# Kernel tuning notes

Hardware: AMD Instinct MI355X
Metric: run time of the kernel (lower is better)

Reference implementation:

```python
import jax, jax.numpy as jnp
import numpy as np

B, T, C, H = 2, 2048, 1024, 16
HD = C // H  # head dim = 64


def setup_inputs() -> dict:
    key = jax.random.key(0)
    ks = jax.random.split(key, 9)
    s = 1.0 / np.sqrt(C)
    return {
        "x": jax.random.normal(ks[0], (B, T, C), dtype=jnp.float32),
        "Wq": jax.random.normal(ks[1], (C, C), dtype=jnp.float32) * s,
        "bq": jax.random.normal(ks[2], (C,), dtype=jnp.float32) * 0.02,
        "Wk": jax.random.normal(ks[3], (C, C), dtype=jnp.float32) * s,
        "bk": jax.random.normal(ks[4], (C,), dtype=jnp.float32) * 0.02,
        "Wv": jax.random.normal(ks[5], (C, C), dtype=jnp.float32) * s,
        "bv": jax.random.normal(ks[6], (C,), dtype=jnp.float32) * 0.02,
        "Wo": jax.random.normal(ks[7], (C, C), dtype=jnp.float32) * s,
        "bo": jax.random.normal(ks[8], (C,), dtype=jnp.float32) * 0.02,
    }


def reference(x, Wq, bq, Wk, bk, Wv, bv, Wo, bo):
    # Projections (torch Linear: x @ W.T + b; here W stored pre-transposed as [C_in, C_out])
    q = x @ Wq + bq  # (B,T,C)
    k = x @ Wk + bk
    v = x @ Wv + bv
    # Split heads: (B,T,C) -> (B,H,T,HD)
    q = q.reshape(B, T, H, HD).transpose(0, 2, 1, 3)
    k = k.reshape(B, T, H, HD).transpose(0, 2, 1, 3)
    v = v.reshape(B, T, H, HD).transpose(0, 2, 1, 3)
    # NOTE: original module never applies a causal mask despite its name.
    score = jnp.einsum("bhqd,bhkd->bhqk", q, k) / jnp.sqrt(jnp.float32(HD))
    score = jax.nn.softmax(score, axis=-1)
    y = jnp.einsum("bhqk,bhkd->bhqd", score, v)
    y = y.transpose(0, 2, 1, 3).reshape(B, T, C)
    # dropout is identity in eval mode
    return y @ Wo + bo
```

## Files before the change

### kernel.cpp

```cpp
#include <hip/hip_runtime.h>
#include <math.h>

#define B_ 2
#define T_ 2048
#define C_ 1024
#define H_ 16
#define HD_ 64
#define M_ (B_*T_)

typedef _Float16 half2v __attribute__((ext_vector_type(2)));
typedef _Float16 half4v __attribute__((ext_vector_type(4)));
typedef _Float16 half8v __attribute__((ext_vector_type(8)));
typedef float f32x4 __attribute__((ext_vector_type(4)));

#define GLD_LDS(gp, lp) \
  __builtin_amdgcn_global_load_lds( \
      (const __attribute__((address_space(1))) void*)(gp), \
      (__attribute__((address_space(3))) void*)(lp), 16, 0, 0)

__global__ __launch_bounds__(256) void cast_f16_kernel(
    const float* __restrict__ src, _Float16* __restrict__ dst, int n4)
{
  int i = blockIdx.x * 256 + threadIdx.x;
  if (i < n4) {
    float4 v = ((const float4*)src)[i];
    half4v h; h[0] = (_Float16)v.x; h[1] = (_Float16)v.y;
    h[2] = (_Float16)v.z; h[3] = (_Float16)v.w;
    ((half4v*)dst)[i] = h;
  }
}

__global__ __launch_bounds__(256) void transpose_cast_all_kernel(
    const float* __restrict__ Wq, const float* __restrict__ Wk,
    const float* __restrict__ Wv, const float* __restrict__ Wo,
    _Float16* __restrict__ Wt3, _Float16* __restrict__ Wot)
{
  const float* W; _Float16* Wt;
  switch (blockIdx.z) {
    case 0:  W = Wq; Wt = Wt3; break;
    case 1:  W = Wk; Wt = Wt3 + (size_t)1024 * 1024; break;
    case 2:  W = Wv; Wt = Wt3 + (size_t)2048 * 1024; break;
    default: W = Wo; Wt = Wot; break;
  }
  __shared__ float tile[32][33];
  const int tx = threadIdx.x, ty = threadIdx.y;
  const int n0 = blockIdx.x * 32, k0 = blockIdx.y * 32;
#pragma unroll
  for (int r = 0; r < 4; r++) {
    int k = ty + r * 8;
    tile[k][tx] = W[(size_t)(k0 + k) * C_ + n0 + tx];
  }
  __syncthreads();
#pragma unroll
  for (int r = 0; r < 4; r++) {
    int n = ty + r * 8;
    Wt[(size_t)(n0 + n) * C_ + k0 + tx] = (_Float16)tile[tx][n];
  }
}

__global__ __launch_bounds__(256) void concat_bias_kernel(
    const float* __restrict__ bq, const float* __restrict__ bk,
    const float* __restrict__ bv, float* __restrict__ b3)
{
  int i = blockIdx.x * 256 + threadIdx.x;
  const float* s = (i < 1024) ? bq : ((i < 2048) ? bk : bv);
  b3[i] = s[i & 1023];
}

template <int BM, int BN, int EPI>
__global__ __launch_bounds__(256) void gemm_f16_kernel(
    const _Float16* __restrict__ A, const _Float16* __restrict__ Bw,
    const float* __restrict__ bias,
    _Float16* __restrict__ o0, _Float16* __restrict__ o1,
    _Float16* __restrict__ o2, float* __restrict__ of)
{
  constexpr int FM = BM / 32, FN = BN / 32;
  __shared__ __align__(16) _Float16 As[BM * 32];
  __shared__ __align__(16) _Float16 Bs[BN * 32];
  const int t = threadIdx.x;
  const int w = t >> 6, lane = t & 63, l15 = lane & 15, quad = lane >> 4;
  const int wm = (w & 1) * (BM / 2), wn = (w >> 1) * (BN / 2);
  const int bm = blockIdx.y * BM, bn = blockIdx.x * BN;
  const int lrow = lane >> 2, lcol = (lane & 3) * 8;

  f32x4 acc[FM][FN];
#pragma unroll
  for (int i = 0; i < FM; i++)
#pragma unroll
    for (int j = 0; j < FN; j++) acc[i][j] = (f32x4){0.f, 0.f, 0.f, 0.f};

  for (int k0 = 0; k0 < 1024; k0 += 32) {
#pragma unroll
    for (int i = 0; i < BM / 64; i++) {
      int ca = w + 4 * i;
      int row = ca * 16 + lrow;
      GLD_LDS(A + (size_t)(bm + row) * 1024 + k0 + lcol, As + ca * 512);
    }
#pragma unroll
    for (int i = 0; i < BN / 64; i++) {
      int cb = w + 4 * i;
      int row = cb * 16 + lrow;
      GLD_LDS(Bw + (size_t)(bn + row) * 1024 + k0 + lcol, Bs + cb * 512);
    }
    __syncthreads();

    half8v af[FM], bf[FN];
#pragma unroll
    for (int mt = 0; mt < FM; mt++)
      af[mt] = *(const half8v*)(As + (wm + mt * 16 + l15) * 32 + quad * 8);
#pragma unroll
    for (int nt = 0; nt < FN; nt++)
      bf[nt] = *(const half8v*)(Bs + (wn + nt * 16 + l15) * 32 + quad * 8);
#pragma unroll
    for (int mt = 0; mt < FM; mt++)
#pragma unroll
      for (int nt = 0; nt < FN; nt++)
        acc[mt][nt] = __builtin_amdgcn_mfma_f32_16x16x32_f16(
            af[mt], bf[nt], acc[mt][nt], 0, 0, 0);
    __syncthreads();
  }

#pragma unroll
  for (int mt = 0; mt < FM; mt++)
#pragma unroll
    for (int nt = 0; nt < FN; nt++) {
      int n = bn + wn + nt * 16 + l15;
      float bv = bias[n];
#pragma unroll
      for (int r = 0; r < 4; r++) {
        int m = bm + wm + mt * 16 + quad * 4 + r;
        float v = acc[mt][nt][r] + bv;
        if (EPI == 0) {
          if (bn < 1024) {
            o0[(size_t)m * 1024 + n] = (_Float16)(v * 0.180336884f);
          } else if (bn < 2048) {
            o1[(size_t)m * 1024 + (n - 1024)] = (_Float16)v;
          } else {
            int dg = n - 2048;
            int hh = dg >> 6, hd = dg & 63;
            int bb = m >> 11, tt = m & 2047;
            o2[(((size_t)(bb * H_ + hh)) * 64 + hd) * 2048 + tt] = (_Float16)v;
          }
        } else {
          of[(size_t)m * 1024 + n] = v;
        }
      }
    }
}

__global__ __launch_bounds__(256) void attn_f16_kernel(
    const _Float16* __restrict__ Qh, const _Float16* __restrict__ Kh,
    const _Float16* __restrict__ Vt, _Float16* __restrict__ Yh)
{
  __shared__ __align__(16) _Float16 Ks[64 * 68];
  __shared__ __align__(16) _Float16 Vs[64 * 68];
  const int t = threadIdx.x;
  const int w = t >> 6, lane = t & 63, l15 = lane & 15, quad = lane >> 4;
  const int qt = blockIdx.x, h = blockIdx.y, b = blockIdx.z;
  const int qg = qt * 64 + w * 16 + l15;
  const size_t qoff = ((size_t)(b * T_ + qg)) * C_ + h * HD_;

  half8v qf[2];
  qf[0] = *(const half8v*)(Qh + qoff + quad * 8);
  qf[1] = *(const half8v*)(Qh + qoff + 32 + quad * 8);

  f32x4 o[4];
#pragma unroll
  for (int i = 0; i < 4; i++) o[i] = (f32x4){0.f, 0.f, 0.f, 0.f};
  float m_run = -INFINITY, l_run = 0.f;

  const size_t kbase = ((size_t)b * T_) * C_ + h * HD_;
  const size_t vbase = ((size_t)(b * H_ + h)) * HD_ * 2048;

  const int srow = t >> 3, scp = t & 7;

  for (int kt0 = 0; kt0 < T_; kt0 += 64) {
#pragma unroll
    for (int i = 0; i < 2; i++) {
      int row = srow + i * 32;
      *(uint4*)((char*)Ks + row * 136 + scp * 16) =
          *(const uint4*)(Kh + kbase + (size_t)(kt0 + row) * C_ + scp * 8);
      *(uint4*)((char*)Vs + row * 136 + scp * 16) =
          *(const uint4*)(Vt + vbase + (size_t)row * 2048 + kt0 + scp * 8);
    }
    __syncthreads();

    f32x4 s[4];
#pragma unroll
    for (int kt = 0; kt < 4; kt++) {
      s[kt] = (f32x4){0.f, 0.f, 0.f, 0.f};
      int key = kt * 16 + l15;
#pragma unroll
      for (int ks = 0; ks < 2; ks++) {
        half8v kf = *(const half8v*)((char*)Ks + key * 136 + (ks * 4 + quad) * 16);
        s[kt] = __builtin_amdgcn_mfma_f32_16x16x32_f16(kf, qf[ks], s[kt], 0, 0, 0);
      }
    }

    float tmax = -INFINITY;
#pragma unroll
    for (int kt = 0; kt < 4; kt++)
#pragma unroll
      for (int r = 0; r < 4; r++) tmax = fmaxf(tmax, s[kt][r]);
    tmax = fmaxf(tmax, __shfl_xor(tmax, 16));
    tmax = fmaxf(tmax, __shfl_xor(tmax, 32));
    float mnew = fmaxf(m_run, tmax);
    float alpha = __builtin_amdgcn_exp2f(m_run - mnew);

    float psum = 0.f;
    half4v pf[4];
#pragma unroll
    for (int kt = 0; kt < 4; kt++) {
      float p0 = __builtin_amdgcn_exp2f(s[kt][0] - mnew);
      float p1 = __builtin_amdgcn_exp2f(s[kt][1] - mnew);
      float p2 = __builtin_amdgcn_exp2f(s[kt][2] - mnew);
      float p3 = __builtin_amdgcn_exp2f(s[kt][3] - mnew);
      psum += (p0 + p1) + (p2 + p3);
      half2v pk01 = __builtin_bit_cast(half2v, __builtin_amdgcn_cvt_pkrtz(p0, p1));
      half2v pk23 = __builtin_bit_cast(half2v, __builtin_amdgcn_cvt_pkrtz(p2, p3));
      pf[kt] = __builtin_shufflevector(pk01, pk23, 0, 1, 2, 3);
    }
    psum += __shfl_xor(psum, 16);
    psum += __shfl_xor(psum, 32);
    l_run = l_run * alpha + psum;
    m_run = mnew;
#pragma unroll
    for (int dt = 0; dt < 4; dt++) o[dt] *= alpha;

#pragma unroll
    for (int dt = 0; dt < 4; dt++) {
      int d = dt * 16 + l15;
#pragma unroll
      for (int kt = 0; kt < 4; kt++) {
        half4v vf = *(const half4v*)((char*)Vs + d * 136 + kt * 32 + quad * 8);
        o[dt] = __builtin_amdgcn_mfma_f32_16x16x16f16(vf, pf[kt], o[dt], 0, 0, 0);
      }
    }
    __syncthreads();
  }

  float inv = 1.0f / l_run;
#pragma unroll
  for (int dt = 0; dt < 4; dt++) {
    half4v yv;
#pragma unroll
    for (int r = 0; r < 4; r++) yv[r] = (_Float16)(o[dt][r] * inv);
    *(half4v*)(Yh + qoff + dt * 16 + quad * 4) = yv;
  }
}

extern "C" void kernel_launch(void* const* d_in, const int* in_sizes, int n_in,
                              void* d_out, int out_size, void* d_ws, size_t ws_size,
                              hipStream_t stream) {
  const float* x  = (const float*)d_in[0];
  const float* Wq = (const float*)d_in[1];
  const float* bq = (const float*)d_in[2];
  const float* Wk = (const float*)d_in[3];
  const float* bk = (const float*)d_in[4];
  const float* Wv = (const float*)d_in[5];
  const float* bv = (const float*)d_in[6];
  const float* Wo = (const float*)d_in[7];
  const float* bo = (const float*)d_in[8];
  float* out = (float*)d_out;

  char* ws = (char*)d_ws;
  _Float16* xh   = (_Float16*)(ws);
  _Float16* Qh   = (_Float16*)(ws + (((size_t)8)  << 20));
  _Float16* Kh   = (_Float16*)(ws + (((size_t)16) << 20));
  _Float16* Vt   = (_Float16*)(ws + (((size_t)24) << 20));
  _Float16* Yh   = (_Float16*)(ws + (((size_t)32) << 20));
  _Float16* Wt3  = (_Float16*)(ws + (((size_t)40) << 20));
  _Float16* Wot  = (_Float16*)(ws + (((size_t)46) << 20));
  float*    b3   = (float*)   (ws + (((size_t)48) << 20));

  cast_f16_kernel<<<(M_ * C_ / 4 + 255) / 256, 256, 0, stream>>>(x, xh, M_ * C_ / 4);
  transpose_cast_all_kernel<<<dim3(32, 32, 4), dim3(32, 8), 0, stream>>>(
      Wq, Wk, Wv, Wo, Wt3, Wot);
  concat_bias_kernel<<<12, 256, 0, stream>>>(bq, bk, bv, b3);

  gemm_f16_kernel<128, 128, 0><<<dim3(24, 32), 256, 0, stream>>>(
      xh, Wt3, b3, Qh, Kh, Vt, nullptr);

  attn_f16_kernel<<<dim3(T_ / 64, H_, B_), 256, 0, stream>>>(Qh, Kh, Vt, Yh);

  gemm_f16_kernel<64, 128, 1><<<dim3(8, 64), 256, 0, stream>>>(
      Yh, Wot, bo, nullptr, nullptr, nullptr, out);
}
```

Before: 223.1 us.

## Double-buffer attention K/V tiles, lazy softmax rescale, separate V transpose kernel

```diff
diff --git a/kernel.cpp b/kernel.cpp
--- a/kernel.cpp
+++ b/kernel.cpp
@@ -65,6 +65,35 @@
   int i = blockIdx.x * 256 + threadIdx.x;
   const float* s = (i < 1024) ? bq : ((i < 2048) ? bk : bv);
   b3[i] = s[i & 1023];
+}
+
+__global__ __launch_bounds__(256) void transpose_v_kernel(
+    const _Float16* __restrict__ Vh, _Float16* __restrict__ Vt)
+{
+  __shared__ __align__(16) _Float16 tile[64 * 64];
+  const int tid = threadIdx.x;
+  const int t0 = blockIdx.x * 64;
+  const int bb = blockIdx.y >> 4, hh = blockIdx.y & 15;
+#pragma unroll
+  for (int i = 0; i < 2; i++) {
+    int slot = tid + i * 256;
+    int row_t = slot >> 3, cp = slot & 7;
+    uint4 v = *(const uint4*)(Vh + (size_t)(bb * T_ + t0 + row_t) * C_ +
+                              hh * 64 + cp * 8);
+    half8v hv = __builtin_bit_cast(half8v, v);
+    int c = ((row_t >> 3) ^ cp) * 8 + (row_t & 7);
+#pragma unroll
+    for (int j = 0; j < 8; j++)
+      tile[(cp * 8 + j) * 64 + c] = hv[j];
+  }
+  __syncthreads();
+#pragma unroll
+  for (int i = 0; i < 2; i++) {
+    int slot = tid + i * 256;
+    int d_row = slot >> 3, tc = slot & 7;
+    uint4 v = *(const uint4*)(tile + d_row * 64 + (tc ^ (d_row >> 3)) * 8);
+    *(uint4*)(Vt + ((size_t)(bb * H_ + hh) * 64 + d_row) * 2048 + t0 + tc * 8) = v;
+  }
 }
 
 template <int BM, int BN, int EPI>
@@ -136,10 +165,7 @@
           } else if (bn < 2048) {
             o1[(size_t)m * 1024 + (n - 1024)] = (_Float16)v;
           } else {
-            int dg = n - 2048;
-            int hh = dg >> 6, hd = dg & 63;
-            int bb = m >> 11, tt = m & 2047;
-            o2[(((size_t)(bb * H_ + hh)) * 64 + hd) * 2048 + tt] = (_Float16)v;
+            o2[(size_t)m * 1024 + (n - 2048)] = (_Float16)v;
           }
         } else {
           of[(size_t)m * 1024 + n] = v;
@@ -152,8 +178,8 @@
     const _Float16* __restrict__ Qh, const _Float16* __restrict__ Kh,
     const _Float16* __restrict__ Vt, _Float16* __restrict__ Yh)
 {
-  __shared__ __align__(16) _Float16 Ks[64 * 68];
-  __shared__ __align__(16) _Float16 Vs[64 * 68];
+  __shared__ __align__(16) _Float16 Ks[2 * 64 * 68];
+  __shared__ __align__(16) _Float16 Vs[2 * 64 * 68];
   const int t = threadIdx.x;
   const int w = t >> 6, lane = t & 63, l15 = lane & 15, quad = lane >> 4;
   const int qt = blockIdx.x, h = blockIdx.y, b = blockIdx.z;
@@ -174,16 +200,36 @@
 
   const int srow = t >> 3, scp = t & 7;
 
+  uint4 pk[2], pv[2];
+#pragma unroll
+  for (int i = 0; i < 2; i++) {
+    int row = srow + i * 32;
+    pk[i] = *(const uint4*)(Kh + kbase + (size_t)row * C_ + scp * 8);
+    pv[i] = *(const uint4*)(Vt + vbase + (size_t)row * 2048 + scp * 8);
+  }
+#pragma unroll
+  for (int i = 0; i < 2; i++) {
+    int row = srow + i * 32;
+    *(uint4*)((char*)Ks + row * 136 + scp * 16) = pk[i];
+    *(uint4*)((char*)Vs + row * 136 + scp * 16) = pv[i];
+  }
+  __syncthreads();
+
   for (int kt0 = 0; kt0 < T_; kt0 += 64) {
-#pragma unroll
-    for (int i = 0; i < 2; i++) {
-      int row = srow + i * 32;
-      *(uint4*)((char*)Ks + row * 136 + scp * 16) =
-          *(const uint4*)(Kh + kbase + (size_t)(kt0 + row) * C_ + scp * 8);
-      *(uint4*)((char*)Vs + row * 136 + scp * 16) =
-          *(const uint4*)(Vt + vbase + (size_t)row * 2048 + kt0 + scp * 8);
-    }
-    __syncthreads();
+    const int cur = (kt0 >> 6) & 1;
+    const char* Ksc = (const char*)(Ks + cur * (64 * 68));
+    const char* Vsc = (const char*)(Vs + cur * (64 * 68));
+    const bool more = (kt0 + 64) < T_;
+
+    if (more) {
+      int kn = kt0 + 64;
+#pragma unroll
+      for (int i = 0; i < 2; i++) {
+        int row = srow + i * 32;
+        pk[i] = *(const uint4*)(Kh + kbase + (size_t)(kn + row) * C_ + scp * 8);
+        pv[i] = *(const uint4*)(Vt + vbase + (size_t)row * 2048 + kn + scp * 8);
+      }
+    }
 
     f32x4 s[4];
 #pragma unroll
@@ -192,7 +238,7 @@
       int key = kt * 16 + l15;
 #pragma unroll
       for (int ks = 0; ks < 2; ks++) {
-        half8v kf = *(const half8v*)((char*)Ks + key * 136 + (ks * 4 + quad) * 16);
+        half8v kf = *(const half8v*)(Ksc + key * 136 + (ks * 4 + quad) * 16);
         s[kt] = __builtin_amdgcn_mfma_f32_16x16x32_f16(kf, qf[ks], s[kt], 0, 0, 0);
       }
     }
@@ -204,17 +250,23 @@
       for (int r = 0; r < 4; r++) tmax = fmaxf(tmax, s[kt][r]);
     tmax = fmaxf(tmax, __shfl_xor(tmax, 16));
     tmax = fmaxf(tmax, __shfl_xor(tmax, 32));
-    float mnew = fmaxf(m_run, tmax);
-    float alpha = __builtin_amdgcn_exp2f(m_run - mnew);
+    if (__any(tmax > m_run)) {
+      float mnew = fmaxf(m_run, tmax);
+      float alpha = __builtin_amdgcn_exp2f(m_run - mnew);
+      l_run *= alpha;
+#pragma unroll
+      for (int dt = 0; dt < 4; dt++) o[dt] *= alpha;
+      m_run = mnew;
+    }
 
     float psum = 0.f;
     half4v pf[4];
 #pragma unroll
     for (int kt = 0; kt < 4; kt++) {
-      float p0 = __builtin_amdgcn_exp2f(s[kt][0] - mnew);
-      float p1 = __builtin_amdgcn_exp2f(s[kt][1] - mnew);
-      float p2 = __builtin_amdgcn_exp2f(s[kt][2] - mnew);
-      float p3 = __builtin_amdgcn_exp2f(s[kt][3] - mnew);
+      float p0 = __builtin_amdgcn_exp2f(s[kt][0] - m_run);
+      float p1 = __builtin_amdgcn_exp2f(s[kt][1] - m_run);
+      float p2 = __builtin_amdgcn_exp2f(s[kt][2] - m_run);
+      float p3 = __builtin_amdgcn_exp2f(s[kt][3] - m_run);
       psum += (p0 + p1) + (p2 + p3);
       half2v pk01 = __builtin_bit_cast(half2v, __builtin_amdgcn_cvt_pkrtz(p0, p1));
       half2v pk23 = __builtin_bit_cast(half2v, __builtin_amdgcn_cvt_pkrtz(p2, p3));
@@ -222,18 +274,26 @@
     }
     psum += __shfl_xor(psum, 16);
     psum += __shfl_xor(psum, 32);
-    l_run = l_run * alpha + psum;
-    m_run = mnew;
-#pragma unroll
-    for (int dt = 0; dt < 4; dt++) o[dt] *= alpha;
+    l_run += psum;
 
 #pragma unroll
     for (int dt = 0; dt < 4; dt++) {
       int d = dt * 16 + l15;
 #pragma unroll
       for (int kt = 0; kt < 4; kt++) {
-        half4v vf = *(const half4v*)((char*)Vs + d * 136 + kt * 32 + quad * 8);
+        half4v vf = *(const half4v*)(Vsc + d * 136 + kt * 32 + quad * 8);
         o[dt] = __builtin_amdgcn_mfma_f32_16x16x16f16(vf, pf[kt], o[dt], 0, 0, 0);
+      }
+    }
+
+    if (more) {
+      char* Ksn = (char*)(Ks + (cur ^ 1) * (64 * 68));
+      char* Vsn = (char*)(Vs + (cur ^ 1) * (64 * 68));
+#pragma unroll
+      for (int i = 0; i < 2; i++) {
+        int row = srow + i * 32;
+        *(uint4*)(Ksn + row * 136 + scp * 16) = pk[i];
+        *(uint4*)(Vsn + row * 136 + scp * 16) = pv[i];
       }
     }
     __syncthreads();
@@ -267,11 +327,12 @@
   _Float16* xh   = (_Float16*)(ws);
   _Float16* Qh   = (_Float16*)(ws + (((size_t)8)  << 20));
   _Float16* Kh   = (_Float16*)(ws + (((size_t)16) << 20));
-  _Float16* Vt   = (_Float16*)(ws + (((size_t)24) << 20));
-  _Float16* Yh   = (_Float16*)(ws + (((size_t)32) << 20));
-  _Float16* Wt3  = (_Float16*)(ws + (((size_t)40) << 20));
-  _Float16* Wot  = (_Float16*)(ws + (((size_t)46) << 20));
-  float*    b3   = (float*)   (ws + (((size_t)48) << 20));
+  _Float16* Vh   = (_Float16*)(ws + (((size_t)24) << 20));
+  _Float16* Vt   = (_Float16*)(ws + (((size_t)32) << 20));
+  _Float16* Yh   = (_Float16*)(ws + (((size_t)40) << 20));
+  _Float16* Wt3  = (_Float16*)(ws + (((size_t)48) << 20));
+  _Float16* Wot  = (_Float16*)(ws + (((size_t)54) << 20));
+  float*    b3   = (float*)   (ws + (((size_t)56) << 20));
 
   cast_f16_kernel<<<(M_ * C_ / 4 + 255) / 256, 256, 0, stream>>>(x, xh, M_ * C_ / 4);
   transpose_cast_all_kernel<<<dim3(32, 32, 4), dim3(32, 8), 0, stream>>>(
@@ -279,7 +340,9 @@
   concat_bias_kernel<<<12, 256, 0, stream>>>(bq, bk, bv, b3);
 
   gemm_f16_kernel<128, 128, 0><<<dim3(24, 32), 256, 0, stream>>>(
-      xh, Wt3, b3, Qh, Kh, Vt, nullptr);
+      xh, Wt3, b3, Qh, Kh, Vh, nullptr);
+
+  transpose_v_kernel<<<dim3(T_ / 64, B_ * H_), 256, 0, stream>>>(Vh, Vt);
 
   attn_f16_kernel<<<dim3(T_ / 64, H_, B_), 256, 0, stream>>>(Qh, Kh, Vt, Yh);
 
```

Measured after the change: 368.3 us. 1.65x slower.
